# Kernel optimization log

Hardware: AMD Instinct MI355X
Metric: run time of the kernel (lower is better)

The kernel has to match this reference:

```python
import jax, jax.numpy as jnp
import numpy as np

DIM = 1024
HID = 2 * DIM
NUM_EXPERTS = 8
TOP_K = 2
BATCH, SEQ = 2, 2048


def setup_inputs() -> dict:
    key = jax.random.key(0)
    ks = jax.random.split(key, 8)
    s = 0.02
    return {
        "x": jax.random.normal(ks[0], (BATCH, SEQ, DIM), jnp.float32),
        "router_w": jax.random.normal(ks[1], (DIM, NUM_EXPERTS), jnp.float32) * s,
        "router_b": jnp.zeros((NUM_EXPERTS,), jnp.float32),
        "sw1": jax.random.normal(ks[2], (DIM, HID), jnp.float32) * s,
        "sb1": jnp.zeros((HID,), jnp.float32),
        "sw2": jax.random.normal(ks[3], (HID, DIM), jnp.float32) * s,
        "sb2": jnp.zeros((DIM,), jnp.float32),
        "ew1": jax.random.normal(ks[4], (NUM_EXPERTS, DIM, HID), jnp.float32) * s,
        "eb1": jnp.zeros((NUM_EXPERTS, HID), jnp.float32),
        "ew2": jax.random.normal(ks[5], (NUM_EXPERTS, HID, DIM), jnp.float32) * s,
        "eb2": jnp.zeros((NUM_EXPERTS, DIM), jnp.float32),
    }


def _gelu(x):
    # torch nn.GELU default is the exact (erf) form
    return jax.nn.gelu(x, approximate=False)


def reference(x, router_w, router_b, sw1, sb1, sw2, sb2, ew1, eb1, ew2, eb2):
    B, S, D = x.shape
    flat = x.reshape(-1, D)                      # [T, D]
    T = flat.shape[0]

    # Router: softmax -> top-k -> renormalize
    probs = jax.nn.softmax(flat @ router_w + router_b, axis=-1)  # [T, E]
    top_w, top_i = jax.lax.top_k(probs, TOP_K)                   # [T, K]
    top_w = top_w / jnp.sum(top_w, axis=-1, keepdims=True)
    # Dense per-token combine weights [T, E] (zero for unrouted experts)
    comb = jnp.zeros_like(probs).at[jnp.arange(T)[:, None], top_i].set(top_w)

    # Shared expert (always on)
    shared = _gelu(flat @ sw1 + sb1) @ sw2 + sb2                 # [T, D]

    # All experts as one batched GEMM pair; zero weights kill unrouted tokens.
    h = _gelu(jnp.einsum('td,edh->eth', flat, ew1) + eb1[:, None, :])  # [E, T, H]
    eo = jnp.einsum('eth,ehd->etd', h, ew2) + eb2[:, None, :]          # [E, T, D]
    moe = jnp.einsum('te,etd->td', comb, eo)                           # [T, D]

    return (shared + moe).reshape(B, S, D)
```

## Files before the change

### kernel.cpp

```cpp
#include <hip/hip_runtime.h>

#define DIM   1024
#define HID   2048
#define NE    8
#define T_TOK 4096

typedef __attribute__((ext_vector_type(8))) short short8;
typedef __attribute__((ext_vector_type(4))) float f32x4;

__device__ __forceinline__ ushort f2bf(float f) {
    union { float f; unsigned u; } v; v.f = f;
    unsigned r = v.u + 0x7FFFu + ((v.u >> 16) & 1u);
    return (ushort)(r >> 16);
}

__device__ __forceinline__ float gelu_fast(float x) {
    float t = x * x;
    float u = x * (1.0f + 0.044715f * t);
    float e = exp2f(2.3020585f * u);
    return x - x / (e + 1.0f);
}

__global__ __launch_bounds__(256)
void transpose_conv18(const float* __restrict__ ew1, const float* __restrict__ sw1,
                      const float* __restrict__ ew2, const float* __restrict__ sw2,
                      ushort* __restrict__ ew1T, ushort* __restrict__ sw1T,
                      ushort* __restrict__ ew2T, ushort* __restrict__ sw2T) {
    __shared__ float tile[64][65];
    int z = blockIdx.z;
    const float* in; ushort* out; int R, C, bx, by;
    if (z < 9) {
        R = DIM; C = HID; bx = blockIdx.x; by = blockIdx.y;
        in  = (z < 8) ? ew1  + (size_t)z * R * C : sw1;
        out = (z < 8) ? ew1T + (size_t)z * R * C : sw1T;
    } else {
        int zz = z - 9;
        R = HID; C = DIM;
        bx = blockIdx.x & 15; by = blockIdx.y * 2 + (blockIdx.x >> 4);
        in  = (zz < 8) ? ew2  + (size_t)zz * R * C : sw2;
        out = (zz < 8) ? ew2T + (size_t)zz * R * C : sw2T;
    }
    int c0 = bx * 64, r0 = by * 64;
    int t = threadIdx.x;
    int lr = t >> 4, lc4 = (t & 15) * 4;
#pragma unroll
    for (int p = 0; p < 4; ++p) {
        float4 f = *(const float4*)(in + (size_t)(r0 + p * 16 + lr) * C + c0 + lc4);
        tile[p * 16 + lr][lc4]     = f.x;
        tile[p * 16 + lr][lc4 + 1] = f.y;
        tile[p * 16 + lr][lc4 + 2] = f.z;
        tile[p * 16 + lr][lc4 + 3] = f.w;
    }
    __syncthreads();
    int oc = t >> 3, rg = (t & 7) * 8;
#pragma unroll
    for (int p = 0; p < 2; ++p) {
        int c = p * 32 + oc;
        short8 o;
#pragma unroll
        for (int j = 0; j < 8; ++j) o[j] = (short)f2bf(tile[rg + j][c]);
        *(short8*)(out + (size_t)(c0 + c) * R + r0 + rg) = o;
    }
}

__global__ void router_kernel(const float* __restrict__ x, const float* __restrict__ rw,
                              const float* __restrict__ rb, int* __restrict__ cnt,
                              int* __restrict__ ids, float* __restrict__ wts,
                              int* __restrict__ te, int* __restrict__ tp,
                              ushort* __restrict__ xb) {
    int wave = threadIdx.x >> 6;
    int lane = threadIdx.x & 63;
    int t = blockIdx.x * 4 + wave;
    const float* xr = x + (size_t)t * DIM;
    ushort* xo = xb + (size_t)t * DIM;
    float acc[NE];
#pragma unroll
    for (int e = 0; e < NE; ++e) acc[e] = 0.f;
    {
        int d0 = lane * 16;
        float v[16];
#pragma unroll
        for (int j = 0; j < 16; j += 4) {
            float4 f = *(const float4*)(xr + d0 + j);
            v[j] = f.x; v[j+1] = f.y; v[j+2] = f.z; v[j+3] = f.w;
        }
        short8 o0, o1;
#pragma unroll
        for (int j = 0; j < 8; ++j) { o0[j] = (short)f2bf(v[j]); o1[j] = (short)f2bf(v[8+j]); }
        *(short8*)(xo + d0)     = o0;
        *(short8*)(xo + d0 + 8) = o1;
#pragma unroll
        for (int j = 0; j < 16; ++j) {
#pragma unroll
            for (int e = 0; e < NE; ++e) acc[e] += v[j] * rw[(d0 + j) * NE + e];
        }
    }
#pragma unroll
    for (int e = 0; e < NE; ++e) {
#pragma unroll
        for (int off = 32; off; off >>= 1) acc[e] += __shfl_xor(acc[e], off);
    }
    if (lane == 0) {
        float l[NE];
#pragma unroll
        for (int e = 0; e < NE; ++e) l[e] = acc[e] + rb[e];
        int i1 = 0;
#pragma unroll
        for (int e = 1; e < NE; ++e) if (l[e] > l[i1]) i1 = e;
        int i2 = (i1 == 0) ? 1 : 0;
#pragma unroll
        for (int e = 0; e < NE; ++e) if (e != i1 && l[e] > l[i2]) i2 = e;
        float p2 = __expf(l[i2] - l[i1]);
        float w1 = 1.0f / (1.0f + p2);
        float w2 = p2 / (1.0f + p2);
        int pos1 = atomicAdd(&cnt[i1], 1);
        ids[i1 * T_TOK + pos1] = t; wts[i1 * T_TOK + pos1] = w1;
        te[2 * t] = i1; tp[2 * t] = pos1;
        int pos2 = atomicAdd(&cnt[i2], 1);
        ids[i2 * T_TOK + pos2] = t; wts[i2 * T_TOK + pos2] = w2;
        te[2 * t + 1] = i2; tp[2 * t + 1] = pos2;
    }
}

__global__ void build_queue(const int* __restrict__ cnt, int* __restrict__ offs,
                            int* __restrict__ q1, int* __restrict__ q2,
                            int* __restrict__ nq) {
    if (threadIdx.x != 0) return;
    int s = 0;
    for (int e = 0; e < NE; ++e) { offs[e] = s; s += cnt[e]; }
    int k1 = 0, k2 = 0;
    for (int z = 0; z <= NE; ++z) {
        int c = (z < NE) ? cnt[z] : T_TOK;
        int mts1 = (c + 127) >> 7;
        for (int mt = 0; mt < mts1; ++mt)
            for (int nt = 0; nt < HID / 128; ++nt)
                q1[k1++] = (z << 16) | (mt << 8) | nt;
        int mts2 = (c + 255) >> 8;
        for (int mt = 0; mt < mts2; ++mt)
            for (int nt = 0; nt < DIM / 256; ++nt)
                q2[k2++] = (z << 16) | (mt << 8) | nt;
    }
    nq[0] = k1; nq[1] = k2;
    nq[2] = 0;  nq[3] = 0;
}

__device__ __forceinline__ void mma_tile(
    const ushort* __restrict__ A, const int* __restrict__ gather, int count,
    const ushort* __restrict__ BT, int K, int tileM, int tileN,
    ushort* lds, f32x4 acc[4][4])
{
    const int tid  = threadIdx.x;
    const int lane = tid & 63, wave = tid >> 6;
    const int g = lane >> 4, fr = lane & 15;
    const int swl = (fr & 7) << 3;
    const int sub = lane >> 3;
    const int kcs = ((lane & 7) ^ sub) << 3;
    const int wr = wave >> 1, wc = wave & 1;

    const ushort* asrc[4];
    const ushort* bsrc[4];
#pragma unroll
    for (int i = 0; i < 4; ++i) {
        int row = (wave * 4 + i) * 8 + sub;
        int ar = tileM + row; if (ar > count - 1) ar = count - 1;
        int grow = gather ? gather[ar] : ar;
        asrc[i] = A  + (size_t)grow * K + kcs;
        bsrc[i] = BT + (size_t)(tileN + row) * K + kcs;
    }

    const int NT = K >> 6;
    for (int t = 0; t < NT; ++t) {
#pragma unroll
        for (int i = 0; i < 4; ++i) {
            int chunk = wave * 4 + i;
            __builtin_amdgcn_global_load_lds(
                (const __attribute__((address_space(1))) void*)(asrc[i] + t * 64),
                (__attribute__((address_space(3))) void*)(lds + chunk * 512),
                16, 0, 0);
            __builtin_amdgcn_global_load_lds(
                (const __attribute__((address_space(1))) void*)(bsrc[i] + t * 64),
                (__attribute__((address_space(3))) void*)(lds + 8192 + chunk * 512),
                16, 0, 0);
        }
        __syncthreads();
#pragma unroll
        for (int kk = 0; kk < 2; ++kk) {
            int koff = (kk * 32 + g * 8) ^ swl;
            short8 a[4], b[4];
#pragma unroll
            for (int m = 0; m < 4; ++m) {
                int row = wr * 64 + m * 16 + fr;
                a[m] = *(const short8*)&lds[row * 64 + koff];
            }
#pragma unroll
            for (int n = 0; n < 4; ++n) {
                int col = wc * 64 + n * 16 + fr;
                b[n] = *(const short8*)&lds[8192 + col * 64 + koff];
            }
#pragma unroll
            for (int m = 0; m < 4; ++m)
#pragma unroll
                for (int n = 0; n < 4; ++n)
                    acc[m][n] = __builtin_amdgcn_mfma_f32_16x16x32_bf16(
                        a[m], b[n], acc[m][n], 0, 0, 0);
        }
        __syncthreads();
    }
}

__device__ __forceinline__ void mma256_k32(
    const ushort* __restrict__ A, int count,
    const ushort* __restrict__ BT, int K, int tileM, int tileN,
    ushort* lds, f32x4 acc[8][4])
{
    const int tid  = threadIdx.x;
    const int lane = tid & 63, wave = tid >> 6;
    const int wr = wave >> 2, wc = wave & 3;
    const int g = lane >> 4, fr = lane & 15;
    const int subr = lane >> 2;
    const int kcs = (((lane & 3) ^ ((lane >> 3) & 3)) << 3);

    const ushort* asrc[2];
    const ushort* bsrc[2];
#pragma unroll
    for (int i = 0; i < 2; ++i) {
        int row = (wave * 2 + i) * 16 + subr;
        int ar = tileM + row; if (ar > count - 1) ar = count - 1;
        asrc[i] = A  + (size_t)ar * K + kcs;
        bsrc[i] = BT + (size_t)(tileN + row) * K + kcs;
    }

    auto STAGE = [&](int buf, int t) {
        ushort* base = lds + buf * 16384;
#pragma unroll
        for (int i = 0; i < 2; ++i) {
            int chunk = wave * 2 + i;
            __builtin_amdgcn_global_load_lds(
                (const __attribute__((address_space(1))) void*)(asrc[i] + t * 32),
                (__attribute__((address_space(3))) void*)(base + chunk * 512),
                16, 0, 0);
            __builtin_amdgcn_global_load_lds(
                (const __attribute__((address_space(1))) void*)(bsrc[i] + t * 32),
                (__attribute__((address_space(3))) void*)(base + 8192 + chunk * 512),
                16, 0, 0);
        }
    };

    auto COMPUTE = [&](int buf) {
        const ushort* A_s = lds + buf * 16384;
        const ushort* B_s = A_s + 8192;
        short8 a[8], b[4];
#pragma unroll
        for (int m = 0; m < 8; ++m) {
            int row = wr * 128 + m * 16 + fr;
            a[m] = *(const short8*)&A_s[row * 32 + ((g ^ ((row >> 1) & 3)) << 3)];
        }
#pragma unroll
        for (int n = 0; n < 4; ++n) {
            int col = wc * 64 + n * 16 + fr;
            b[n] = *(const short8*)&B_s[col * 32 + ((g ^ ((col >> 1) & 3)) << 3)];
        }
#pragma unroll
        for (int m = 0; m < 8; ++m)
#pragma unroll
            for (int n = 0; n < 4; ++n)
                acc[m][n] = __builtin_amdgcn_mfma_f32_16x16x32_bf16(
                    a[m], b[n], acc[m][n], 0, 0, 0);
    };

    const int NT = K >> 5;
    STAGE(0, 0);
    STAGE(1, 1);
    STAGE(2, 2);
    for (int t = 0; t < NT; ++t) {
        if (t + 3 < NT) {
            STAGE((t + 3) & 3, t + 3);
            asm volatile("s_waitcnt vmcnt(12)" ::: "memory");
        } else {
            int rem = NT - 1 - t;
            if (rem == 2)      asm volatile("s_waitcnt vmcnt(8)" ::: "memory");
            else if (rem == 1) asm volatile("s_waitcnt vmcnt(4)" ::: "memory");
            else               asm volatile("s_waitcnt vmcnt(0)" ::: "memory");
        }
        __builtin_amdgcn_s_barrier();
        asm volatile("" ::: "memory");
        COMPUTE(t & 3);
        asm volatile("" ::: "memory");
        __builtin_amdgcn_s_barrier();
    }
}

__global__ __launch_bounds__(256, 4)
void gemm1_kernel(const ushort* __restrict__ xb,
                  const ushort* __restrict__ ew1T, const ushort* __restrict__ sw1T,
                  const float* __restrict__ eb1, const float* __restrict__ sb1,
                  const int* __restrict__ ids, const int* __restrict__ cnt,
                  const int* __restrict__ offs,
                  const int* __restrict__ q1, const int* __restrict__ nq,
                  int* __restrict__ qc, ushort* __restrict__ h)
{
    __shared__ ushort lds[16384];
    __shared__ int s_it;
    const int nit = nq[0];
    const int lane = threadIdx.x & 63, wave = threadIdx.x >> 6;
    const int wr = wave >> 1, wc = wave & 1, g = lane >> 4, fr = lane & 15;

    for (;;) {
        if (threadIdx.x == 0) s_it = atomicAdd(qc, 1);
        __syncthreads();
        int it = s_it;
        if (it >= nit) break;
        int item = q1[it];
        int z = item >> 16, mt = (item >> 8) & 255, nt = item & 255;
        int count, hbase;
        const ushort* BT; const float* bias; const int* gather;
        if (z < NE) {
            count  = cnt[z];
            BT     = ew1T + (size_t)z * HID * DIM;
            bias   = eb1 + z * HID;
            gather = ids + z * T_TOK;
            hbase  = T_TOK + offs[z];
        } else {
            count = T_TOK; BT = sw1T; bias = sb1; gather = nullptr; hbase = 0;
        }
        int tileM = mt * 128, tileN = nt * 128;

        f32x4 acc[4][4];
#pragma unroll
        for (int m = 0; m < 4; ++m)
#pragma unroll
            for (int n = 0; n < 4; ++n) acc[m][n] = (f32x4){0.f, 0.f, 0.f, 0.f};

        mma_tile(xb, gather, count, BT, DIM, tileM, tileN, lds, acc);

#pragma unroll
        for (int n = 0; n < 4; ++n) {
            int col = tileN + wc * 64 + n * 16 + fr;
            float bc = bias[col];
#pragma unroll
            for (int m = 0; m < 4; ++m) {
#pragma unroll
                for (int i = 0; i < 4; ++i) {
                    int row = tileM + wr * 64 + m * 16 + g * 4 + i;
                    if (row < count)
                        h[(size_t)(hbase + row) * HID + col] =
                            f2bf(gelu_fast(acc[m][n][i] + bc));
                }
            }
        }
    }
}

__global__ __launch_bounds__(512, 1)
void gemm2_kernel(const ushort* __restrict__ h,
                  const ushort* __restrict__ ew2T, const ushort* __restrict__ sw2T,
                  const float* __restrict__ eb2, const float* __restrict__ sb2,
                  const float* __restrict__ wts,
                  const int* __restrict__ cnt, const int* __restrict__ offs,
                  const int* __restrict__ q2, const int* __restrict__ n2,
                  float* __restrict__ eo, float* __restrict__ out)
{
    extern __shared__ ushort lds[];
    const int nit = *n2;
    const int lane = threadIdx.x & 63, wave = threadIdx.x >> 6;
    const int wr = wave >> 2, wc = wave & 3, g = lane >> 4, fr = lane & 15;

    for (int it = blockIdx.x; it < nit; it += gridDim.x) {
        int item = q2[it];
        int z = item >> 16, mt = (item >> 8) & 255, nt = item & 255;
        int count;
        const ushort* BT; const float* bias; const float* tw; float* dst;
        const ushort* Arows;
        if (z < NE) {
            count = cnt[z];
            BT    = ew2T + (size_t)z * DIM * HID;
            bias  = eb2 + z * DIM;
            tw    = wts + z * T_TOK;
            Arows = h + (size_t)(T_TOK + offs[z]) * HID;
            dst   = eo + (size_t)offs[z] * DIM;
        } else {
            count = T_TOK; BT = sw2T; bias = sb2; tw = nullptr;
            Arows = h;
            dst   = out;
        }
        int tileM = mt * 256, tileN = nt * 256;

        f32x4 acc[8][4];
#pragma unroll
        for (int m = 0; m < 8; ++m)
#pragma unroll
            for (int n = 0; n < 4; ++n) acc[m][n] = (f32x4){0.f, 0.f, 0.f, 0.f};

        mma256_k32(Arows, count, BT, HID, tileM, tileN, lds, acc);

#pragma unroll
        for (int m = 0; m < 8; ++m) {
#pragma unroll
            for (int i = 0; i < 4; ++i) {
                int row = tileM + wr * 128 + m * 16 + g * 4 + i;
                if (row < count) {
                    float w = tw ? tw[row] : 1.0f;
#pragma unroll
                    for (int n = 0; n < 4; ++n) {
                        int col = tileN + wc * 64 + n * 16 + fr;
                        dst[(size_t)row * DIM + col] = w * (acc[m][n][i] + bias[col]);
                    }
                }
            }
        }
        __syncthreads();
    }
}

__global__ void combine_kernel(const float* __restrict__ eo, const int* __restrict__ te,
                               const int* __restrict__ tp, const int* __restrict__ offs,
                               float* __restrict__ out)
{
    int t = blockIdx.x;
    int s1 = offs[te[2 * t]]     + tp[2 * t];
    int s2 = offs[te[2 * t + 1]] + tp[2 * t + 1];
    int d = threadIdx.x * 4;
    float4 a = *(const float4*)(out + (size_t)t * DIM + d);
    float4 b = *(const float4*)(eo + (size_t)s1 * DIM + d);
    float4 c = *(const float4*)(eo + (size_t)s2 * DIM + d);
    a.x += b.x + c.x; a.y += b.y + c.y; a.z += b.z + c.z; a.w += b.w + c.w;
    *(float4*)(out + (size_t)t * DIM + d) = a;
}

extern "C" void kernel_launch(void* const* d_in, const int* in_sizes, int n_in,
                              void* d_out, int out_size, void* d_ws, size_t ws_size,
                              hipStream_t stream)
{
    const float* x   = (const float*)d_in[0];
    const float* rw  = (const float*)d_in[1];
    const float* rb  = (const float*)d_in[2];
    const float* sw1 = (const float*)d_in[3];
    const float* sb1 = (const float*)d_in[4];
    const float* sw2 = (const float*)d_in[5];
    const float* sb2 = (const float*)d_in[6];
    const float* ew1 = (const float*)d_in[7];
    const float* eb1 = (const float*)d_in[8];
    const float* ew2 = (const float*)d_in[9];
    const float* eb2 = (const float*)d_in[10];
    float* out = (float*)d_out;

    char* p = (char*)d_ws;
    ushort* xb   = (ushort*)p;  p += (size_t)T_TOK * DIM * 2;
    ushort* sw1T = (ushort*)p;  p += (size_t)HID * DIM * 2;
    ushort* sw2T = (ushort*)p;  p += (size_t)DIM * HID * 2;
    ushort* ew1T = (ushort*)p;  p += (size_t)NE * HID * DIM * 2;
    ushort* ew2T = (ushort*)p;  p += (size_t)NE * DIM * HID * 2;
    ushort* hbuf = (ushort*)p;  p += (size_t)(3 * T_TOK) * HID * 2;
    float*  eo   = (float*)p;   p += (size_t)(2 * T_TOK) * DIM * 4;
    int*    ids  = (int*)p;     p += (size_t)NE * T_TOK * 4;
    float*  wts  = (float*)p;   p += (size_t)NE * T_TOK * 4;
    int*    te   = (int*)p;     p += (size_t)2 * T_TOK * 4;
    int*    tp   = (int*)p;     p += (size_t)2 * T_TOK * 4;
    int*    cnt  = (int*)p;     p += 256;
    int*    offs = (int*)p;     p += 256;
    int*    q1   = (int*)p;     p += 16384;
    int*    q2   = (int*)p;     p += 8192;
    int*    nq   = (int*)p;     p += 256;

    hipFuncSetAttribute((const void*)gemm2_kernel,
                        hipFuncAttributeMaxDynamicSharedMemorySize, 131072);

    hipMemsetAsync(cnt, 0, 256, stream);

    router_kernel<<<dim3(T_TOK / 4), 256, 0, stream>>>(x, rw, rb, cnt, ids, wts, te, tp, xb);
    transpose_conv18<<<dim3(32, 16, 18), 256, 0, stream>>>(
        ew1, sw1, ew2, sw2, ew1T, sw1T, ew2T, sw2T);
    build_queue<<<dim3(1), 64, 0, stream>>>(cnt, offs, q1, q2, nq);
    gemm1_kernel<<<dim3(1024), 256, 0, stream>>>(
        xb, ew1T, sw1T, eb1, sb1, ids, cnt, offs, q1, nq, nq + 2, hbuf);
    gemm2_kernel<<<dim3(256), 512, 131072, stream>>>(
        hbuf, ew2T, sw2T, eb2, sb2, wts, cnt, offs, q2, nq + 1, eo, out);
    combine_kernel<<<dim3(T_TOK), 256, 0, stream>>>(eo, te, tp, offs, out);
}
```

Before: 346.6 us.

## Load gemm2 B operand directly to registers, stage only A through LDS

Replaces the shared 4-stage LDS pipeline in gemm2 with a double-buffered scheme. Only the A tile (K=64 per stage, XOR-swizzled) goes through LDS via global_load_lds, while each wave loads its B fragments straight from global memory into registers with inline global_load_dwordx4. This halves LDS use to 64KB and cuts LDS traffic and bank pressure for B. The cost is more register pressure, a shallower prefetch depth, and B reads that are not shared across waves in the same column.

```diff
diff --git a/kernel.cpp b/kernel.cpp
--- a/kernel.cpp
+++ b/kernel.cpp
@@ -208,88 +208,6 @@
     }
 }
 
-__device__ __forceinline__ void mma256_k32(
-    const ushort* __restrict__ A, int count,
-    const ushort* __restrict__ BT, int K, int tileM, int tileN,
-    ushort* lds, f32x4 acc[8][4])
-{
-    const int tid  = threadIdx.x;
-    const int lane = tid & 63, wave = tid >> 6;
-    const int wr = wave >> 2, wc = wave & 3;
-    const int g = lane >> 4, fr = lane & 15;
-    const int subr = lane >> 2;
-    const int kcs = (((lane & 3) ^ ((lane >> 3) & 3)) << 3);
-
-    const ushort* asrc[2];
-    const ushort* bsrc[2];
-#pragma unroll
-    for (int i = 0; i < 2; ++i) {
-        int row = (wave * 2 + i) * 16 + subr;
-        int ar = tileM + row; if (ar > count - 1) ar = count - 1;
-        asrc[i] = A  + (size_t)ar * K + kcs;
-        bsrc[i] = BT + (size_t)(tileN + row) * K + kcs;
-    }
-
-    auto STAGE = [&](int buf, int t) {
-        ushort* base = lds + buf * 16384;
-#pragma unroll
-        for (int i = 0; i < 2; ++i) {
-            int chunk = wave * 2 + i;
-            __builtin_amdgcn_global_load_lds(
-                (const __attribute__((address_space(1))) void*)(asrc[i] + t * 32),
-                (__attribute__((address_space(3))) void*)(base + chunk * 512),
-                16, 0, 0);
-            __builtin_amdgcn_global_load_lds(
-                (const __attribute__((address_space(1))) void*)(bsrc[i] + t * 32),
-                (__attribute__((address_space(3))) void*)(base + 8192 + chunk * 512),
-                16, 0, 0);
-        }
-    };
-
-    auto COMPUTE = [&](int buf) {
-        const ushort* A_s = lds + buf * 16384;
-        const ushort* B_s = A_s + 8192;
-        short8 a[8], b[4];
-#pragma unroll
-        for (int m = 0; m < 8; ++m) {
-            int row = wr * 128 + m * 16 + fr;
-            a[m] = *(const short8*)&A_s[row * 32 + ((g ^ ((row >> 1) & 3)) << 3)];
-        }
-#pragma unroll
-        for (int n = 0; n < 4; ++n) {
-            int col = wc * 64 + n * 16 + fr;
-            b[n] = *(const short8*)&B_s[col * 32 + ((g ^ ((col >> 1) & 3)) << 3)];
-        }
-#pragma unroll
-        for (int m = 0; m < 8; ++m)
-#pragma unroll
-            for (int n = 0; n < 4; ++n)
-                acc[m][n] = __builtin_amdgcn_mfma_f32_16x16x32_bf16(
-                    a[m], b[n], acc[m][n], 0, 0, 0);
-    };
-
-    const int NT = K >> 5;
-    STAGE(0, 0);
-    STAGE(1, 1);
-    STAGE(2, 2);
-    for (int t = 0; t < NT; ++t) {
-        if (t + 3 < NT) {
-            STAGE((t + 3) & 3, t + 3);
-            asm volatile("s_waitcnt vmcnt(12)" ::: "memory");
-        } else {
-            int rem = NT - 1 - t;
-            if (rem == 2)      asm volatile("s_waitcnt vmcnt(8)" ::: "memory");
-            else if (rem == 1) asm volatile("s_waitcnt vmcnt(4)" ::: "memory");
-            else               asm volatile("s_waitcnt vmcnt(0)" ::: "memory");
-        }
-        __builtin_amdgcn_s_barrier();
-        asm volatile("" ::: "memory");
-        COMPUTE(t & 3);
-        asm volatile("" ::: "memory");
-        __builtin_amdgcn_s_barrier();
-    }
-}
-
 __global__ __launch_bounds__(256, 4)
 void gemm1_kernel(const ushort* __restrict__ xb,
                   const ushort* __restrict__ ew1T, const ushort* __restrict__ sw1T,
@@ -351,7 +269,7 @@
     }
 }
 
-__global__ __launch_bounds__(512, 1)
+__global__ __launch_bounds__(512)
 void gemm2_kernel(const ushort* __restrict__ h,
                   const ushort* __restrict__ ew2T, const ushort* __restrict__ sw2T,
                   const float* __restrict__ eb2, const float* __restrict__ sb2,
@@ -363,7 +281,12 @@
     extern __shared__ ushort lds[];
     const int nit = *n2;
     const int lane = threadIdx.x & 63, wave = threadIdx.x >> 6;
-    const int wr = wave >> 2, wc = wave & 3, g = lane >> 4, fr = lane & 15;
+    const int wr = wave >> 2, wc = wave & 3;
+    const int g = lane >> 4, fr = lane & 15;
+    const int swl = (fr & 7) << 3;
+    const int sub = lane >> 3;
+    const int kcs = ((lane & 7) ^ sub) << 3;
+    const int K = HID;
 
     for (int it = blockIdx.x; it < nit; it += gridDim.x) {
         int item = q2[it];
@@ -391,7 +314,88 @@
 #pragma unroll
             for (int n = 0; n < 4; ++n) acc[m][n] = (f32x4){0.f, 0.f, 0.f, 0.f};
 
-        mma256_k32(Arows, count, BT, HID, tileM, tileN, lds, acc);
+        const ushort* asrc[4];
+#pragma unroll
+        for (int i = 0; i < 4; ++i) {
+            int row = (wave * 4 + i) * 8 + sub;
+            int ar = tileM + row; if (ar > count - 1) ar = count - 1;
+            asrc[i] = Arows + (size_t)ar * K + kcs;
+        }
+        auto STAGE_A = [&](int buf, int t) {
+            ushort* base = lds + buf * 16384;
+#pragma unroll
+            for (int i = 0; i < 4; ++i) {
+                int chunk = wave * 4 + i;
+                __builtin_amdgcn_global_load_lds(
+                    (const __attribute__((address_space(1))) void*)(asrc[i] + t * 64),
+                    (__attribute__((address_space(3))) void*)(base + chunk * 512),
+                    16, 0, 0);
+            }
+        };
+
+        unsigned voff[8];
+#pragma unroll
+        for (int kk = 0; kk < 2; ++kk)
+#pragma unroll
+            for (int n = 0; n < 4; ++n) {
+                int col = wc * 64 + n * 16 + fr;
+                voff[kk * 4 + n] = (unsigned)(((tileN + col) * K + kk * 32 + g * 8) * 2);
+            }
+        short8 b0[8], b1[8];
+        auto LOADB = [&](short8 (&B)[8]) {
+#pragma unroll
+            for (int q = 0; q < 8; ++q) {
+                asm volatile("global_load_dwordx4 %0, %1, %2"
+                             : "=v"(B[q]) : "v"(voff[q]), "s"(BT) : "memory");
+                voff[q] += 128;
+            }
+        };
+
+        auto COMPUTE = [&](const ushort* A_s, short8 (&b)[8]) {
+#pragma unroll
+            for (int kk = 0; kk < 2; ++kk) {
+                int koff = (kk * 32 + g * 8) ^ swl;
+                short8 a[8];
+#pragma unroll
+                for (int m = 0; m < 8; ++m) {
+                    int row = wr * 128 + m * 16 + fr;
+                    a[m] = *(const short8*)&A_s[row * 64 + koff];
+                }
+#pragma unroll
+                for (int m = 0; m < 8; ++m)
+#pragma unroll
+                    for (int n = 0; n < 4; ++n)
+                        acc[m][n] = __builtin_amdgcn_mfma_f32_16x16x32_bf16(
+                            a[m], b[kk * 4 + n], acc[m][n], 0, 0, 0);
+            }
+        };
+
+        const int NT = K >> 6;
+        STAGE_A(0, 0);
+        LOADB(b0);
+        for (int t = 0; t < NT; t += 2) {
+            if (t + 1 < NT) {
+                STAGE_A(1, t + 1); LOADB(b1);
+                asm volatile("s_waitcnt vmcnt(12)" ::: "memory");
+            } else {
+                asm volatile("s_waitcnt vmcnt(0)" ::: "memory");
+            }
+            __builtin_amdgcn_s_barrier();
+            __builtin_amdgcn_sched_barrier(0);
+            COMPUTE(lds, b0);
+            __builtin_amdgcn_s_barrier();
+            if (t + 1 >= NT) break;
+            if (t + 2 < NT) {
+                STAGE_A(0, t + 2); LOADB(b0);
+                asm volatile("s_waitcnt vmcnt(12)" ::: "memory");
+            } else {
+                asm volatile("s_waitcnt vmcnt(0)" ::: "memory");
+            }
+            __builtin_amdgcn_s_barrier();
+            __builtin_amdgcn_sched_barrier(0);
+            COMPUTE(lds + 16384, b1);
+            __builtin_amdgcn_s_barrier();
+        }
 
 #pragma unroll
         for (int m = 0; m < 8; ++m) {
@@ -463,7 +467,7 @@
     int*    nq   = (int*)p;     p += 256;
 
     hipFuncSetAttribute((const void*)gemm2_kernel,
-                        hipFuncAttributeMaxDynamicSharedMemorySize, 131072);
+                        hipFuncAttributeMaxDynamicSharedMemorySize, 65536);
 
     hipMemsetAsync(cnt, 0, 256, stream);
 
@@ -473,7 +477,7 @@
     build_queue<<<dim3(1), 64, 0, stream>>>(cnt, offs, q1, q2, nq);
     gemm1_kernel<<<dim3(1024), 256, 0, stream>>>(
         xb, ew1T, sw1T, eb1, sb1, ids, cnt, offs, q1, nq, nq + 2, hbuf);
-    gemm2_kernel<<<dim3(256), 512, 131072, stream>>>(
+    gemm2_kernel<<<dim3(256), 512, 65536, stream>>>(
         hbuf, ew2T, sw2T, eb2, sb2, wts, cnt, offs, q2, nq + 1, eo, out);
     combine_kernel<<<dim3(T_TOK), 256, 0, stream>>>(eo, te, tp, offs, out);
 }
```

Result: slower. 437.1 us (+26.1%).
